# Kernel optimization log

Hardware: AMD Instinct MI355X
Metric: run time of the kernel (lower is better)

## Reference

```python
import jax, jax.numpy as jnp
import numpy as np

B, N, D, L = 64, 2047, 512, 4
T = D + 1        # token_dim = d + 1
H = 512          # hidden_dim
LN_EPS = 1e-5
ATTN_EPS = 1e-6


def setup_inputs() -> dict:
    key = jax.random.key(0)
    ks = jax.random.split(key, 10)
    s = 0.01  # matches xavier_uniform_ gain=0.01 small-init magnitude
    return dict(
        xs=jax.random.normal(ks[0], (B, N, D), jnp.float32),
        ys=jax.random.normal(ks[1], (B, N), jnp.float32),
        query_x=jax.random.normal(ks[2], (B, 1, D), jnp.float32),
        Wq=jax.random.normal(ks[3], (L, H, T), jnp.float32) * s,
        Wk=jax.random.normal(ks[4], (L, H, T), jnp.float32) * s,
        Wv=jax.random.normal(ks[5], (L, T, T), jnp.float32) * s,
        Wo=jax.random.normal(ks[6], (L, T, T), jnp.float32) * s,
        ln1_w=jnp.ones((L, T), jnp.float32),
        ln1_b=jnp.zeros((L, T), jnp.float32),
        ln2_w=jnp.ones((L, T), jnp.float32),
        ln2_b=jnp.zeros((L, T), jnp.float32),
        scale=jnp.ones((L,), jnp.float32),
        pred_w=jax.random.normal(ks[7], (1, T), jnp.float32) * 0.02,
    )


def _ln(x, w, b):
    m = jnp.mean(x, axis=-1, keepdims=True)
    v = jnp.var(x, axis=-1, keepdims=True)
    return (x - m) * jax.lax.rsqrt(v + LN_EPS) * w + b


def _l2norm(x):
    n = jnp.sqrt(jnp.sum(x * x, axis=-1, keepdims=True))
    return x / jnp.maximum(n, 1e-12)


def _forward(xs, ys, query_x, Wq, Wk, Wv, Wo, ln1_w, ln1_b, ln2_w, ln2_b, scale, pred_w):
    b = xs.shape[0]
    train_tokens = jnp.concatenate([xs, ys[..., None]], axis=-1)          # [B,N,T]
    query_token = jnp.concatenate([query_x, jnp.zeros((b, 1, 1), xs.dtype)], axis=-1)
    tokens = jnp.concatenate([train_tokens, query_token], axis=1)          # [B,N+1,T]

    def step(tok, p):
        wq, wk, wv, wo, w1, b1, w2, b2, sc = p
        x = _ln(tok, w1, b1)
        Q = jnp.einsum('bnt,ht->bnh', x, wq)
        K = jnp.einsum('bnt,ht->bnh', x, wk)
        V = jnp.einsum('bnt,ut->bnu', x, wv)
        Q = _l2norm(Q)
        K = _l2norm(K)
        s = jax.nn.softplus(sc)
        Qp = (jax.nn.elu(Q) + 1.0) * s
        Kp = jax.nn.elu(K) + 1.0
        KV = jnp.einsum('bnh,bnu->bhu', Kp, V)      # [B,H,T]
        Ksum = jnp.sum(Kp, axis=1)                  # [B,H]
        denom = jnp.einsum('bnh,bh->bn', Qp, Ksum)  # [B,N+1]
        attn = jnp.einsum('bnh,bhu->bnu', Qp, KV) / (denom[..., None] + ATTN_EPS)
        out = jnp.einsum('bnu,tu->bnt', attn, wo) * 0.1 + tok
        return _ln(out, w2, b2), None

    tokens, _ = jax.lax.scan(step, tokens, (Wq, Wk, Wv, Wo, ln1_w, ln1_b, ln2_w, ln2_b, scale))
    q_out = tokens[:, -1, :]                        # [B,T]
    return jnp.einsum('bt,ot->bo', q_out, pred_w)[..., 0]  # [B]


def reference(xs, ys, query_x, Wq, Wk, Wv, Wo, ln1_w, ln1_b, ln2_w, ln2_b, scale, pred_w):
    return _forward(xs, ys, query_x, Wq, Wk, Wv, Wo, ln1_w, ln1_b, ln2_w, ln2_b, scale, pred_w)
```

## Files before the change

kernel.cpp:

```cpp
#include <hip/hip_runtime.h>
#include <cstdint>
#include <cstddef>


typedef unsigned short u16;
typedef float f32x4 __attribute__((ext_vector_type(4)));
typedef unsigned short u16x8 __attribute__((ext_vector_type(8)));

#define P 576
#define NQK 1664
#define VTROWS 514
#define KVLD 640

__device__ __forceinline__ float bf2f(u16 s) {
    union { unsigned u; float f; } v; v.u = ((unsigned)s) << 16; return v.f;
}
__device__ __forceinline__ u16 f2bf(float f) {
    union { float f; unsigned u; } v; v.f = f;
    unsigned r = v.u + 0x7FFF + ((v.u >> 16) & 1);
    return (u16)(r >> 16);
}
__device__ __forceinline__ float wredsum(float v) {
#pragma unroll
    for (int o = 32; o > 0; o >>= 1) v += __shfl_xor(v, o, 64);
    return v;
}
__device__ __forceinline__ f32x4 mfma_16x16x32_bf16(u16x8 a, u16x8 b, f32x4 c) {
    asm volatile("v_mfma_f32_16x16x32_bf16 %0, %1, %2, %0"
                 : "+v"(c) : "v"(a), "v"(b));
    return c;
}
__device__ __forceinline__ void gload_lds16(const u16* g, u16* l) {
    __builtin_amdgcn_global_load_lds(
        (const __attribute__((address_space(1))) void*)g,
        (__attribute__((address_space(3))) void*)l, 16, 0, 0);
}

__global__ __launch_bounds__(256) void k_build_tokens(
    const float* __restrict__ xs, const float* __restrict__ ys,
    const float* __restrict__ qx, u16* __restrict__ tok,
    float* __restrict__ meanb, float* __restrict__ rstdb)
{
    long row = (long)blockIdx.x * 4 + (threadIdx.x >> 6);
    int lane = threadIdx.x & 63;
    int b = (int)(row >> 11), n = (int)(row & 2047);
    const float* src = (n < 2047) ? xs + ((long)(b * 2047 + n)) * 512
                                  : qx + (long)b * 512;
    float4 f0 = *(const float4*)(src + lane * 8);
    float4 f1 = *(const float4*)(src + lane * 8 + 4);
    float y = (n < 2047) ? ys[(long)b * 2047 + n] : 0.f;
    float v[8] = {f0.x, f0.y, f0.z, f0.w, f1.x, f1.y, f1.z, f1.w};
    float s = 0.f, sq = 0.f;
#pragma unroll
    for (int j = 0; j < 8; j++) { s += v[j]; sq += v[j] * v[j]; }
    if (lane == 0) { s += y; sq += y * y; }
    s = wredsum(s); sq = wredsum(sq);
    u16x8 o;
#pragma unroll
    for (int j = 0; j < 8; j++) o[j] = f2bf(v[j]);
    *(u16x8*)(tok + row * P + lane * 8) = o;
    if (lane < 8) {
        u16x8 z8 = {0,0,0,0,0,0,0,0};
        if (lane == 0) z8[0] = f2bf(y);
        *(u16x8*)(tok + row * P + 512 + lane * 8) = z8;
    }
    if (lane == 0) {
        float m = s * (1.f / 513.f);
        float var = sq * (1.f / 513.f) - m * m;
        meanb[row] = m;
        rstdb[row] = 1.f / sqrtf(var + 1e-5f);
    }
}

__global__ __launch_bounds__(256) void k_prep_wcat(
    const float* __restrict__ wq, const float* __restrict__ wk,
    const float* __restrict__ wv, const float* __restrict__ ln1w,
    u16* __restrict__ wcat)
{
    long idx = (long)blockIdx.x * 256 + threadIdx.x;
    if (idx >= 4L * NQK * P) return;
    int t = (int)(idx % P);
    long rem = idx / P;
    int r = (int)(rem % NQK);
    int l = (int)(rem / NQK);
    float v = 0.f;
    if (t < 513) {
        float wsc = ln1w[l * 513 + t];
        if (r < 512)       v = wq[((long)l * 512 + r) * 513 + t] * wsc;
        else if (r < 1024) v = wk[((long)l * 512 + (r - 512)) * 513 + t] * wsc;
        else if (r < 1537) v = wv[((long)l * 513 + (r - 1024)) * 513 + t] * wsc;
    }
    wcat[idx] = f2bf(v);
}

__global__ __launch_bounds__(256) void k_prep_wo(
    const float* __restrict__ wo, u16* __restrict__ wop)
{
    long idx = (long)blockIdx.x * 256 + threadIdx.x;
    if (idx >= 4L * P * P) return;
    int u = (int)(idx % P);
    long rem = idx / P;
    int t = (int)(rem % P);
    int l = (int)(rem / P);
    float v = (t < 513 && u < 513) ? wo[((long)l * 513 + t) * 513 + u] : 0.f;
    wop[idx] = f2bf(v);
}

__global__ __launch_bounds__(256) void k_prep_sums(
    const float* __restrict__ wq, const float* __restrict__ wk,
    const float* __restrict__ wv, const float* __restrict__ ln1w,
    const float* __restrict__ ln1b, float* __restrict__ s1, float* __restrict__ s2)
{
    int id = blockIdx.x * 4 + (threadIdx.x >> 6);
    int lane = threadIdx.x & 63;
    int l = id / NQK, r = id % NQK;
    float a1 = 0.f, a2 = 0.f;
    for (int t = lane; t < 513; t += 64) {
        float wc = 0.f;
        if (r < 512)       wc = wq[((long)l * 512 + r) * 513 + t];
        else if (r < 1024) wc = wk[((long)l * 512 + (r - 512)) * 513 + t];
        else if (r < 1537) wc = wv[((long)l * 513 + (r - 1024)) * 513 + t];
        a1 += ln1w[l * 513 + t] * wc;
        a2 += ln1b[l * 513 + t] * wc;
    }
    a1 = wredsum(a1); a2 = wredsum(a2);
    if (lane == 0) { s1[id] = a1; s2[id] = a2; }
}

__global__ __launch_bounds__(256) void k_ln2(
    const u16* __restrict__ z, u16* __restrict__ tok,
    const float* __restrict__ w, const float* __restrict__ bia,
    float* __restrict__ meanb, float* __restrict__ rstdb)
{
    long row = (long)blockIdx.x * 4 + (threadIdx.x >> 6);
    int lane = threadIdx.x & 63;
    const u16* zp = z + row * P;
    u16* tp = tok + row * P;
    u16x8 a0 = *(const u16x8*)(zp + lane * 8);
    u16x8 a1 = {0,0,0,0,0,0,0,0};
    if (lane < 8) a1 = *(const u16x8*)(zp + 512 + lane * 8);
    float v0[8], v1[8];
#pragma unroll
    for (int j = 0; j < 8; j++) v0[j] = bf2f(a0[j]);
#pragma unroll
    for (int j = 0; j < 8; j++) v1[j] = (lane < 8) ? bf2f(a1[j]) : 0.f;
    float s = 0.f, sq = 0.f;
#pragma unroll
    for (int j = 0; j < 8; j++) { s += v0[j]; sq += v0[j] * v0[j]; }
#pragma unroll
    for (int j = 0; j < 8; j++) { s += v1[j]; sq += v1[j] * v1[j]; }
    s = wredsum(s); sq = wredsum(sq);
    float mean = s * (1.f / 513.f);
    float var = sq * (1.f / 513.f) - mean * mean;
    float rstd = 1.f / sqrtf(var + 1e-5f);
    float so = 0.f, so2 = 0.f;
    u16x8 o0;
    float of0[8];
#pragma unroll
    for (int j = 0; j < 8; j++) {
        int t = lane * 8 + j;
        of0[j] = (v0[j] - mean) * rstd * w[t] + bia[t];
        so += of0[j]; so2 += of0[j] * of0[j];
        o0[j] = f2bf(of0[j]);
    }
    float of1[8];
#pragma unroll
    for (int j = 0; j < 8; j++) {
        int t = 512 + lane * 8 + j;
        float ov = 0.f;
        if (lane < 8 && t < 513) ov = (v1[j] - mean) * rstd * w[t] + bia[t];
        of1[j] = ov;
        so += ov; so2 += ov * ov;
    }
    so = wredsum(so); so2 = wredsum(so2);
    *(u16x8*)(tp + lane * 8) = o0;
    if (lane < 8) {
        u16x8 o1;
#pragma unroll
        for (int j = 0; j < 8; j++) o1[j] = f2bf(of1[j]);
        *(u16x8*)(tp + 512 + lane * 8) = o1;
    }
    if (lane == 0) {
        float m2 = so * (1.f / 513.f);
        float v2 = so2 * (1.f / 513.f) - m2 * m2;
        meanb[row] = m2;
        rstdb[row] = 1.f / sqrtf(v2 + 1e-5f);
    }
}

__global__ __launch_bounds__(256) void k_qknorm(
    u16* __restrict__ qkv, float* __restrict__ rkout,
    const float* __restrict__ scale, int l)
{
    long row = (long)blockIdx.x * 4 + (threadIdx.x >> 6);
    int lane = threadIdx.x & 63;
    float s = log1pf(expf(scale[l]));
    u16* rowp = qkv + row * NQK;
    u16x8 q8 = *(const u16x8*)(rowp + lane * 8);
    u16x8 k8 = *(const u16x8*)(rowp + 512 + lane * 8);
    float qf[8];
    float sqv = 0.f, skv = 0.f;
#pragma unroll
    for (int j = 0; j < 8; j++) { qf[j] = bf2f(q8[j]); sqv += qf[j] * qf[j]; }
#pragma unroll
    for (int j = 0; j < 8; j++) { float kf = bf2f(k8[j]); skv += kf * kf; }
    sqv = wredsum(sqv); skv = wredsum(skv);
    float rnq = 1.f / fmaxf(sqrtf(sqv), 1e-12f);
    float rnk = 1.f / fmaxf(sqrtf(skv), 1e-12f);
    u16x8 o;
#pragma unroll
    for (int j = 0; j < 8; j++) {
        float q = qf[j] * rnq;
        float qp = (q > 0.f) ? (q + 1.f) : expf(q);
        o[j] = f2bf(qp * s);
    }
    *(u16x8*)(rowp + lane * 8) = o;
    if (lane == 0) rkout[row] = rnk;
}

__global__ __launch_bounds__(256) void k_trans(
    const u16* __restrict__ qkv, const float* __restrict__ rk,
    u16* __restrict__ kpt)
{
    int ct = blockIdx.x;
    long r0 = (long)blockIdx.y * 64;
    int b = (int)(r0 >> 11);
    int nloc = (int)(r0 & 2047);
    int tid = threadIdx.x;
    int r = tid >> 2;
    int c0 = (tid & 3) * 16;
    __shared__ u16 T[64 * 80];
    const u16* src = qkv + (r0 + r) * NQK + 512 + ct * 64 + c0;
    u16x8 a = *(const u16x8*)src;
    u16x8 d = *(const u16x8*)(src + 8);
    float rkv = rk[r0 + r];
#pragma unroll
    for (int j = 0; j < 8; j++) {
        float kv = bf2f(a[j]) * rkv; kv = (kv > 0.f) ? kv + 1.f : expf(kv);
        T[(c0 + j) * 80 + r] = f2bf(kv);
    }
#pragma unroll
    for (int j = 0; j < 8; j++) {
        float kv = bf2f(d[j]) * rkv; kv = (kv > 0.f) ? kv + 1.f : expf(kv);
        T[(c0 + 8 + j) * 80 + r] = f2bf(kv);
    }
    __syncthreads();
    int orow = tid >> 2;
    int oc0 = (tid & 3) * 16;
    u16x8 w0 = *(const u16x8*)&T[orow * 80 + oc0];
    u16x8 w1 = *(const u16x8*)&T[orow * 80 + oc0 + 8];
    u16* dst = kpt + ((long)b * 512 + ct * 64 + orow) * 2048 + nloc + oc0;
    *(u16x8*)dst = w0;
    *(u16x8*)(dst + 8) = w1;
}

__global__ __launch_bounds__(512) void k_extract_ksum(
    const u16* __restrict__ kvh, float* __restrict__ ksum)
{
    int b = blockIdx.x, h = threadIdx.x;
    ksum[(long)b * 512 + h] = bf2f(kvh[((long)b * 512 + h) * KVLD + 513]);
}

__global__ __launch_bounds__(256) void k_denom(
    const u16* __restrict__ qkv, const float* __restrict__ ksum,
    float* __restrict__ denom)
{
    long row = (long)blockIdx.x * 4 + (threadIdx.x >> 6);
    int lane = threadIdx.x & 63;
    int b = (int)(row >> 11);
    u16x8 q = *(const u16x8*)(qkv + row * NQK + lane * 8);
    const float* ks = ksum + (long)b * 512 + lane * 8;
    float acc = 0.f;
#pragma unroll
    for (int j = 0; j < 8; j++) acc += bf2f(q[j]) * ks[j];
    acc = wredsum(acc);
    if (lane == 0) denom[row] = acc;
}

__global__ void k_predict(const u16* __restrict__ tok, const float* __restrict__ pw,
                          float* __restrict__ out)
{
    int b = blockIdx.x;
    int lane = threadIdx.x;
    const u16* rp = tok + ((long)b * 2048 + 2047) * P;
    float acc = 0.f;
    for (int t = lane; t < 513; t += 64) acc += bf2f(rp[t]) * pw[t];
    acc = wredsum(acc);
    if (lane == 0) out[b] = acc;
}

#define QN 1664

#define QSTAGE(DB, HALF, K0)                                                   \
    {                                                                          \
        _Pragma("unroll")                                                      \
        for (int j = 0; j < 2; j++) {                                          \
            int row_ = j * 64 + srow;                                          \
            const u16* src_;                                                   \
            if ((HALF) < 2) {                                                  \
                src_ = Ag + (long)(m0 + (HALF) * 128 + row_) * 576 + (K0) + colsw; \
            } else {                                                           \
                int gc_ = n0 + ((HALF) - 2) * 128 + row_;                      \
                if (gc_ >= QN) gc_ = QN - 1;                                   \
                src_ = Bg + (long)gc_ * 576 + (K0) + colsw;                    \
            }                                                                  \
            gload_lds16(src_, S + (DB) * 32768 + (HALF) * 8192 + j * 4096 + w * 512); \
        }                                                                      \
    }

#define QLDA(AH)                                                               \
    _Pragma("unroll")                                                          \
    for (int m_ = 0; m_ < 4; m_++) {                                           \
        int rr_ = wr * 64 + m_ * 16 + (lane & 15);                             \
        _Pragma("unroll")                                                      \
        for (int ks_ = 0; ks_ < 2; ks_++)                                      \
            af[m_][ks_] = *(const u16x8*)&Bc[(AH) * 8192 + rr_ * 64 +          \
                          ((ks_ * 32 + (lane >> 4) * 8) ^ swz)];               \
    }

#define QLDB(BH)                                                               \
    _Pragma("unroll")                                                          \
    for (int n_ = 0; n_ < 2; n_++) {                                           \
        int cc_ = wc * 32 + n_ * 16 + (lane & 15);                             \
        _Pragma("unroll")                                                      \
        for (int ks_ = 0; ks_ < 2; ks_++)                                      \
            bf[n_][ks_] = *(const u16x8*)&Bc[16384 + (BH) * 8192 + cc_ * 64 +  \
                          ((ks_ * 32 + (lane >> 4) * 8) ^ swz)];               \
    }

#define QPHASE(AH, BH, RDA, RDB, SHALF)                                        \
    __builtin_amdgcn_sched_barrier(0);                                         \
    if (RDA) { QLDA(AH) }                                                      \
    if (RDB) { QLDB(BH) }                                                      \
    QSTAGE(nb, SHALF, k1)                                                      \
    asm volatile("s_waitcnt vmcnt(4)" ::: "memory");                           \
    __builtin_amdgcn_s_barrier();                                              \
    __builtin_amdgcn_s_setprio(1);                                             \
    _Pragma("unroll")                                                          \
    for (int m_ = 0; m_ < 4; m_++)                                             \
        _Pragma("unroll")                                                      \
        for (int n_ = 0; n_ < 2; n_++) {                                       \
            acc[AH][BH][m_][n_] =                                              \
                mfma_16x16x32_bf16(af[m_][0], bf[n_][0], acc[AH][BH][m_][n_]); \
            acc[AH][BH][m_][n_] =                                              \
                mfma_16x16x32_bf16(af[m_][1], bf[n_][1], acc[AH][BH][m_][n_]); \
        }                                                                      \
    __builtin_amdgcn_s_setprio(0);                                             \
    __builtin_amdgcn_s_barrier();

__global__ __launch_bounds__(512, 2) void k_qkv8(
    const u16* __restrict__ Ag, const u16* __restrict__ Bg, u16* __restrict__ C,
    const float* __restrict__ meanb, const float* __restrict__ rstdb,
    const float* __restrict__ s1l, const float* __restrict__ s2l,
    u16* __restrict__ VT)
{
    extern __shared__ u16 S[];
    int id = blockIdx.x;
    int lin = (id & 7) * 448 + (id >> 3);
    int mt = lin / 7, nt = lin - mt * 7;
    int m0 = mt * 256, n0 = nt * 256;
    int tid = threadIdx.x, lane = tid & 63, w = tid >> 6;
    int wr = w >> 2, wc = w & 3;

    float* auxp = (float*)(S + 65536);
    if (tid < 256) {
        auxp[tid] = meanb[(long)m0 + tid];
        auxp[256 + tid] = rstdb[(long)m0 + tid];
    } else {
        int t = tid - 256;
        int gc = n0 + t; if (gc >= QN) gc = QN - 1;
        auxp[512 + t] = s1l[gc];
        auxp[768 + t] = s2l[gc];
    }

    int srow = (w << 3) + (lane >> 3);
    int colsw = ((lane & 7) << 3) ^ ((lane >> 3) << 3);
    int swz = (lane & 7) << 3;

    f32x4 acc[2][2][4][2];
#pragma unroll
    for (int a_ = 0; a_ < 2; a_++)
#pragma unroll
    for (int b_ = 0; b_ < 2; b_++)
#pragma unroll
    for (int m_ = 0; m_ < 4; m_++)
#pragma unroll
    for (int n_ = 0; n_ < 2; n_++) {
        acc[a_][b_][m_][n_][0] = 0.f; acc[a_][b_][m_][n_][1] = 0.f;
        acc[a_][b_][m_][n_][2] = 0.f; acc[a_][b_][m_][n_][3] = 0.f;
    }
    u16x8 af[4][2], bf[2][2];

    QSTAGE(0, 0, 0) QSTAGE(0, 2, 0) QSTAGE(0, 3, 0) QSTAGE(0, 1, 0)
    asm volatile("s_waitcnt vmcnt(4)" ::: "memory");
    __builtin_amdgcn_s_barrier();

    for (int kt = 0; kt < 9; ++kt) {
        u16* Bc = S + (kt & 1) * 32768;
        int nb = (kt & 1) ^ 1;
        int k1 = (kt >= 8 ? 8 : kt + 1) * 64;
        QPHASE(0, 0, 1, 1, 0)
        QPHASE(0, 1, 0, 1, 2)
        QPHASE(1, 1, 1, 0, 3)
        QPHASE(1, 0, 0, 1, 1)
    }
    asm volatile("s_waitcnt vmcnt(0)" ::: "memory");
    __builtin_amdgcn_s_barrier();

    if (n0 < 1024) {
#pragma unroll
        for (int ah = 0; ah < 2; ah++)
#pragma unroll
        for (int bh = 0; bh < 2; bh++)
#pragma unroll
        for (int m_ = 0; m_ < 4; m_++)
#pragma unroll
        for (int n_ = 0; n_ < 2; n_++) {
            int lr0 = ah * 128 + wr * 64 + m_ * 16 + ((lane >> 4) << 2);
            int lc = bh * 128 + wc * 32 + n_ * 16 + (lane & 15);
            float s1c = auxp[512 + lc], s2c = auxp[768 + lc];
#pragma unroll
            for (int r_ = 0; r_ < 4; r_++) {
                int lr = lr0 + r_;
                float v = auxp[256 + lr] * (acc[ah][bh][m_][n_][r_]
                          - auxp[lr] * s1c) + s2c;
                S[lr * 256 + (lc ^ ((lr & 7) << 3))] = f2bf(v);
            }
        }
        __syncthreads();
#pragma unroll
        for (int i = 0; i < 16; i++) {
            int g = i * 512 + tid;
            int row = g >> 5, c0 = (g & 31) * 8;
            *(u16x8*)&C[(long)(m0 + row) * 1664 + n0 + c0] =
                *(const u16x8*)&S[row * 256 + (c0 ^ ((row & 7) << 3))];
        }
    } else {
        int u0 = n0 - 1024, b = m0 >> 11, nloc = m0 & 2047;
#pragma unroll
        for (int ah = 0; ah < 2; ah++)
#pragma unroll
        for (int bh = 0; bh < 2; bh++)
#pragma unroll
        for (int m_ = 0; m_ < 4; m_++)
#pragma unroll
        for (int n_ = 0; n_ < 2; n_++) {
            int lr0 = ah * 128 + wr * 64 + m_ * 16 + ((lane >> 4) << 2);
            int lc = bh * 128 + wc * 32 + n_ * 16 + (lane & 15);
            float s1c = auxp[512 + lc], s2c = auxp[768 + lc];
#pragma unroll
            for (int r_ = 0; r_ < 4; r_++) {
                int lr = lr0 + r_;
                float v = auxp[256 + lr] * (acc[ah][bh][m_][n_][r_]
                          - auxp[lr] * s1c) + s2c;
                S[lc * 256 + (lr ^ ((lc & 7) << 3))] = f2bf(v);
            }
        }
        __syncthreads();
        const u16x8 ones = {0x3F80,0x3F80,0x3F80,0x3F80,0x3F80,0x3F80,0x3F80,0x3F80};
#pragma unroll
        for (int i = 0; i < 16; i++) {
            int g = i * 512 + tid;
            int ur = g >> 5, t0 = (g & 31) * 8;
            int u = u0 + ur;
            if (u < VTROWS) {
                u16x8 vv;
                if (u == 513) vv = ones;
                else vv = *(const u16x8*)&S[ur * 256 + (t0 ^ ((ur & 7) << 3))];
                *(u16x8*)&VT[((long)b * VTROWS + u) * 2048 + nloc + t0] = vv;
            }
        }
    }
}

__global__ __launch_bounds__(256) void k_gemm_bt(
    const u16* __restrict__ A, const u16* __restrict__ Bt, u16* __restrict__ C,
    int M, int N, int K, int lda, int ldb, int ldc,
    long sA, long sB, long sC,
    const float* __restrict__ aux1, const float* __restrict__ aux2,
    const float* __restrict__ aux3, const float* __restrict__ aux4,
    long sAux, const u16* __restrict__ Res,
    float cscale, int mode, int r1, int padw,
    int ntm, int ntn, int nbz,
    u16* __restrict__ VT, int vtbase)
{
    int G = ntm * ntn * nbz;
    int id = blockIdx.x;
    int lin = (id & 7) * (G >> 3) + (id >> 3);
    int per = ntm * ntn;
    int bz = lin / per;
    int rem = lin - bz * per;
    int mt = rem / ntn;
    int nt = rem - mt * ntn;
    int m0 = mt * 128, n0 = nt * 128;

    A += (long)bz * sA; Bt += (long)bz * sB; C += (long)bz * sC;
    int tid = threadIdx.x, lane = tid & 63, w = tid >> 6;
    int wr = w >> 1, wc = w & 1;
    __shared__ u16 ldsbuf[2 * 128 * 64];
    u16* Als = ldsbuf;
    u16* Bls = ldsbuf + 128 * 64;
    __shared__ float auxR0[128], auxR1[128], auxA1[128];
    __shared__ float auxC0[128], auxC1[128], auxB1[128];

    if (tid < 128) {
        int gr = m0 + tid; if (gr >= M) gr = M - 1;
        float r0v = cscale, r1v = 0.f, a1v = 0.f;
        if (mode == 1) {
            const float* d1 = aux1 + (long)bz * sAux;
            r0v = cscale / (d1[gr] + 1e-6f);
        } else if (mode == 3) { r0v = aux1[gr]; r1v = aux2[gr]; }
        if (r1) a1v = bf2f(A[(long)gr * lda + K]);
        auxR0[tid] = r0v; auxR1[tid] = r1v; auxA1[tid] = a1v;
    } else {
        int t = tid - 128;
        int gc = n0 + t; if (gc >= N) gc = N - 1;
        float c0v = 0.f, c1v = 0.f, b1v = 0.f;
        if (mode == 3) { c0v = aux3[gc]; c1v = aux4[gc]; }
        if (r1) b1v = bf2f(Bt[(long)gc * ldb + K]);
        auxC0[t] = c0v; auxC1[t] = c1v; auxB1[t] = b1v;
    }

    f32x4 acc[4][4];
#pragma unroll
    for (int m = 0; m < 4; m++)
#pragma unroll
        for (int n = 0; n < 4; n++) { acc[m][n][0]=0.f; acc[m][n][1]=0.f; acc[m][n][2]=0.f; acc[m][n][3]=0.f; }

    int srow = lane >> 3;
    int scol = (lane & 7) * 8;
    int scolsw = scol ^ (srow << 3);
    int swz = (lane & 7) << 3;

    for (int k0 = 0; k0 < K; k0 += 64) {
#pragma unroll
        for (int i = 0; i < 4; i++) {
            int rt = (w * 4 + i) * 8 + srow;
            int gr = m0 + rt; gr = (gr < M) ? gr : (M - 1);
            gload_lds16(A + (long)gr * lda + k0 + scolsw, &Als[(w * 4 + i) * 512]);
        }
#pragma unroll
        for (int i = 0; i < 4; i++) {
            int rt = (w * 4 + i) * 8 + srow;
            int gc = n0 + rt; gc = (gc < N) ? gc : (N - 1);
            gload_lds16(Bt + (long)gc * ldb + k0 + scolsw, &Bls[(w * 4 + i) * 512]);
        }
        __syncthreads();
#pragma unroll
        for (int ks = 0; ks < 2; ks++) {
            u16x8 af[4], bfv[4];
#pragma unroll
            for (int m = 0; m < 4; m++) {
                int row = wr * 64 + m * 16 + (lane & 15);
                af[m] = *(const u16x8*)&Als[row * 64 + ((ks * 32 + (lane >> 4) * 8) ^ swz)];
            }
#pragma unroll
            for (int n = 0; n < 4; n++) {
                int col = wc * 64 + n * 16 + (lane & 15);
                bfv[n] = *(const u16x8*)&Bls[col * 64 + ((ks * 32 + (lane >> 4) * 8) ^ swz)];
            }
#pragma unroll
            for (int m = 0; m < 4; m++)
#pragma unroll
                for (int n = 0; n < 4; n++)
                    acc[m][n] = mfma_16x16x32_bf16(af[m], bfv[n], acc[m][n]);
        }
        __syncthreads();
    }

    bool isvt = (VT != nullptr) && (n0 >= vtbase);

    if (Res) {
        const u16* Rp = Res + (long)bz * sC;
#pragma unroll
        for (int i = 0; i < 8; i++) {
            int lrow = i * 16 + (tid >> 4);
            int lcol = (tid & 15) * 8;
            long gr = m0 + lrow; if (gr > (long)M - 1) gr = M - 1;
            long gcol = (long)n0 + lcol;
            long mx = (long)ldc - 8; if (gcol > mx) gcol = mx;
            *(u16x8*)&ldsbuf[lrow * 128 + lcol] = *(const u16x8*)&Rp[gr * ldc + gcol];
        }
        __syncthreads();
    }

    asm volatile("s_nop 7\n\ts_nop 7" ::: );

    if (!isvt) {
#pragma unroll
        for (int m = 0; m < 4; m++) {
            int lrbase = wr * 64 + m * 16 + ((lane >> 4) << 2);
#pragma unroll
            for (int n = 0; n < 4; n++) {
                int lc = wc * 64 + n * 16 + (lane & 15);
                float c0v = auxC0[lc], c1v = auxC1[lc], b1v = auxB1[lc];
#pragma unroll
                for (int r = 0; r < 4; r++) {
                    int lr = lrbase + r;
                    float wv = acc[m][n][r] + auxA1[lr] * b1v;
                    float v;
                    if (mode == 3) v = auxR1[lr] * (wv - auxR0[lr] * c0v) + c1v;
                    else {
                        v = wv * auxR0[lr];
                        if (Res) v += bf2f(ldsbuf[lr * 128 + lc]);
                    }
                    ldsbuf[lr * 128 + lc] = f2bf(v);
                }
            }
        }
        __syncthreads();

        int lcol = (tid & 15) * 8;
        int gc0 = n0 + lcol;
        bool colok = padw || (gc0 + 8 <= N);
#pragma unroll
        for (int i = 0; i < 8; i++) {
            int lrow = i * 16 + (tid >> 4);
            int gr = m0 + lrow;
            if (gr < M && colok) {
                *(u16x8*)&C[(long)gr * ldc + gc0] = *(const u16x8*)&ldsbuf[lrow * 128 + lcol];
            }
        }
    } else {
        int u0 = n0 - vtbase;
        int b = m0 >> 11;
        int nloc = m0 & 2047;
#pragma unroll
        for (int m = 0; m < 4; m++) {
            int lrbase = wr * 64 + m * 16 + ((lane >> 4) << 2);
#pragma unroll
            for (int n = 0; n < 4; n++) {
                int lc = wc * 64 + n * 16 + (lane & 15);
                float c0v = auxC0[lc], c1v = auxC1[lc];
#pragma unroll
                for (int r = 0; r < 4; r++) {
                    int lr = lrbase + r;
                    float wv = acc[m][n][r];
                    float v = (mode == 3) ? (auxR1[lr] * (wv - auxR0[lr] * c0v) + c1v)
                                          : (wv * auxR0[lr]);
                    ldsbuf[lc * 128 + (lr ^ ((lc & 7) << 3))] = f2bf(v);
                }
            }
        }
        __syncthreads();

        int nc = (tid & 15) * 8;
        const u16x8 ones = {0x3F80,0x3F80,0x3F80,0x3F80,0x3F80,0x3F80,0x3F80,0x3F80};
#pragma unroll
        for (int i = 0; i < 8; i++) {
            int ur = i * 16 + (tid >> 4);
            int u = u0 + ur;
            if (u < VTROWS) {
                u16x8 vv;
                if (u == 513) vv = ones;
                else vv = *(const u16x8*)&ldsbuf[ur * 128 + (nc ^ ((ur & 7) << 3))];
                *(u16x8*)&VT[((long)b * VTROWS + u) * 2048 + nloc + nc] = vv;
            }
        }
    }
}

extern "C" void kernel_launch(void* const* d_in, const int* in_sizes, int n_in,
                              void* d_out, int out_size, void* d_ws, size_t ws_size,
                              hipStream_t stream)
{
    const float* xs    = (const float*)d_in[0];
    const float* ys    = (const float*)d_in[1];
    const float* qx    = (const float*)d_in[2];
    const float* Wq    = (const float*)d_in[3];
    const float* Wk    = (const float*)d_in[4];
    const float* Wv    = (const float*)d_in[5];
    const float* Wo    = (const float*)d_in[6];
    const float* ln1w  = (const float*)d_in[7];
    const float* ln1b  = (const float*)d_in[8];
    const float* ln2w  = (const float*)d_in[9];
    const float* ln2b  = (const float*)d_in[10];
    const float* scale = (const float*)d_in[11];
    const float* predw = (const float*)d_in[12];
    float* out = (float*)d_out;

    char* ws = (char*)d_ws;
    u16*   tok   = (u16*)(ws + 0L);
    u16*   buf1  = (u16*)(ws + 150994944L);
    u16*   qkv   = (u16*)(ws + 301989888L);
    u16*   kpt   = (u16*)(ws + 738197504L);
    u16*   kvh   = (u16*)(ws + 872415232L);
    float* denom = (float*)(ws + 914358272L);
    float* meanb = (float*)(ws + 914882560L);
    float* rstdb = (float*)(ws + 915406848L);
    float* ksum  = (float*)(ws + 915931136L);
    u16*   wcat  = (u16*)(ws + 916062208L);
    u16*   wop   = (u16*)(ws + 923729920L);
    float* s1    = (float*)(ws + 926384128L);
    float* s2    = (float*)(ws + 926410752L);
    float* rkb   = (float*)(ws + 301465600L);
    u16*   w2t   = kpt;

    static bool attr_done = false;
    if (!attr_done) {
        (void)hipFuncSetAttribute((const void*)k_qkv8,
            hipFuncAttributeMaxDynamicSharedMemorySize, 135168);
        attr_done = true;
    }

    k_build_tokens<<<32768, 256, 0, stream>>>(xs, ys, qx, tok, meanb, rstdb);
    {
        long n1 = 4L * NQK * P;
        k_prep_wcat<<<(int)((n1 + 255) / 256), 256, 0, stream>>>(Wq, Wk, Wv, ln1w, wcat);
        long n2 = 4L * P * P;
        k_prep_wo<<<(int)((n2 + 255) / 256), 256, 0, stream>>>(Wo, wop);
        k_prep_sums<<<1664, 256, 0, stream>>>(Wq, Wk, Wv, ln1w, ln1b, s1, s2);
    }

    for (int l = 0; l < 4; l++) {
        k_qkv8<<<3584, 512, 135168, stream>>>(tok, wcat + (long)l * NQK * P, qkv,
            meanb, rstdb, s1 + l * NQK, s2 + l * NQK, buf1);
        k_qknorm<<<32768, 256, 0, stream>>>(qkv, rkb, scale, l);
        {
            dim3 g(8, 2048, 1);
            k_trans<<<g, 256, 0, stream>>>(qkv, rkb, kpt);
        }
        k_gemm_bt<<<1280, 256, 0, stream>>>(kpt, buf1, kvh,
            512, VTROWS, 2048, 2048, 2048, KVLD,
            512L * 2048, (long)VTROWS * 2048, 512L * KVLD,
            nullptr, nullptr, nullptr, nullptr, 0, nullptr, 1.f, 0, 0, 1,
            4, 5, 64, nullptr, 1 << 30);
        k_extract_ksum<<<64, 512, 0, stream>>>(kvh, ksum);
        k_denom<<<32768, 256, 0, stream>>>(qkv, ksum, denom);
        k_gemm_bt<<<1280, 256, 0, stream>>>(wop + (long)l * P * P, kvh, w2t,
            576, 512, 512, P, KVLD, 512,
            0, 512L * KVLD, 576L * 512,
            nullptr, nullptr, nullptr, nullptr, 0, nullptr, 1.f, 0, 1, 0,
            5, 4, 64, nullptr, 1 << 30);
        k_gemm_bt<<<5120, 256, 0, stream>>>(qkv, w2t, buf1,
            2048, P, 512, NQK, 512, P,
            2048L * NQK, 576L * 512, 2048L * P,
            denom, nullptr, nullptr, nullptr, 2048, tok,
            0.1f, 1, 0, 0, 16, 5, 64, nullptr, 1 << 30);
        k_ln2<<<32768, 256, 0, stream>>>(buf1, tok, ln2w + l * 513, ln2b + l * 513,
                                         meanb, rstdb);
    }
    k_predict<<<64, 64, 0, stream>>>(tok, predw, out);
}
```

Baseline: 3.494 ms.

## Software-pipeline LDS fragment loads ahead of MFMA phases in QKV GEMM

Restructures the QKV GEMM main loop so LDS reads of the next A/B fragments are issued before or after the MFMA batches, using separate register sets (afA/afB, b0a/b0b). This hides LDS latency behind MFMA work, and the loop is manually unrolled by two tiles to alternate buffers. It costs more VGPRs for the extra fragment arrays, which could cause spills or lower occupancy under launch_bounds(512,2). It also adds lgkmcnt waits before each barrier.

```diff
diff --git a/kernel.cpp b/kernel.cpp
--- a/kernel.cpp
+++ b/kernel.cpp
@@ -308,45 +308,56 @@
         }                                                                      \
     }
 
-#define QLDA(AH)                                                               \
-    _Pragma("unroll")                                                          \
-    for (int m_ = 0; m_ < 4; m_++) {                                           \
-        int rr_ = wr * 64 + m_ * 16 + (lane & 15);                             \
-        _Pragma("unroll")                                                      \
-        for (int ks_ = 0; ks_ < 2; ks_++)                                      \
-            af[m_][ks_] = *(const u16x8*)&Bc[(AH) * 8192 + rr_ * 64 +          \
-                          ((ks_ * 32 + (lane >> 4) * 8) ^ swz)];               \
-    }
-
-#define QLDB(BH)                                                               \
-    _Pragma("unroll")                                                          \
-    for (int n_ = 0; n_ < 2; n_++) {                                           \
-        int cc_ = wc * 32 + n_ * 16 + (lane & 15);                             \
-        _Pragma("unroll")                                                      \
-        for (int ks_ = 0; ks_ < 2; ks_++)                                      \
-            bf[n_][ks_] = *(const u16x8*)&Bc[16384 + (BH) * 8192 + cc_ * 64 +  \
-                          ((ks_ * 32 + (lane >> 4) * 8) ^ swz)];               \
-    }
-
-#define QPHASE(AH, BH, RDA, RDB, SHALF)                                        \
-    __builtin_amdgcn_sched_barrier(0);                                         \
-    if (RDA) { QLDA(AH) }                                                      \
-    if (RDB) { QLDB(BH) }                                                      \
-    QSTAGE(nb, SHALF, k1)                                                      \
-    asm volatile("s_waitcnt vmcnt(4)" ::: "memory");                           \
-    __builtin_amdgcn_s_barrier();                                              \
+#define QLGKM0 asm volatile("s_waitcnt lgkmcnt(0)" ::: "memory");
+#define QVM4   asm volatile("s_waitcnt vmcnt(4)" ::: "memory");
+#define QBAR   __builtin_amdgcn_s_barrier();                                   \
+               __builtin_amdgcn_sched_barrier(0);
+
+#define QMFMA(AF, BF, AH, BH)                                                  \
     __builtin_amdgcn_s_setprio(1);                                             \
     _Pragma("unroll")                                                          \
     for (int m_ = 0; m_ < 4; m_++)                                             \
         _Pragma("unroll")                                                      \
         for (int n_ = 0; n_ < 2; n_++) {                                       \
             acc[AH][BH][m_][n_] =                                              \
-                mfma_16x16x32_bf16(af[m_][0], bf[n_][0], acc[AH][BH][m_][n_]); \
+                mfma_16x16x32_bf16(AF[m_][0], BF[n_][0], acc[AH][BH][m_][n_]); \
             acc[AH][BH][m_][n_] =                                              \
-                mfma_16x16x32_bf16(af[m_][1], bf[n_][1], acc[AH][BH][m_][n_]); \
+                mfma_16x16x32_bf16(AF[m_][1], BF[n_][1], acc[AH][BH][m_][n_]); \
         }                                                                      \
-    __builtin_amdgcn_s_setprio(0);                                             \
-    __builtin_amdgcn_s_barrier();
+    __builtin_amdgcn_s_setprio(0);
+
+#define QLDAF(DST, BUF, AHALF)                                                 \
+    _Pragma("unroll")                                                          \
+    for (int m_ = 0; m_ < 4; m_++) {                                           \
+        int rr_ = wr * 64 + m_ * 16 + (lane & 15);                             \
+        _Pragma("unroll")                                                      \
+        for (int ks_ = 0; ks_ < 2; ks_++)                                      \
+            DST[m_][ks_] = *(const u16x8*)&S[(BUF) * 32768 + (AHALF) * 8192 +  \
+                rr_ * 64 + ((ks_ * 32 + (lane >> 4) * 8) ^ swz)];              \
+    }
+
+#define QLDBF(DST, BUF, BHALF)                                                 \
+    _Pragma("unroll")                                                          \
+    for (int n_ = 0; n_ < 2; n_++) {                                           \
+        int cc_ = wc * 32 + n_ * 16 + (lane & 15);                             \
+        _Pragma("unroll")                                                      \
+        for (int ks_ = 0; ks_ < 2; ks_++)                                      \
+            DST[n_][ks_] = *(const u16x8*)&S[(BUF) * 32768 + 16384 +           \
+                (BHALF) * 8192 + cc_ * 64 + ((ks_ * 32 + (lane >> 4) * 8) ^ swz)]; \
+    }
+
+#define QTILE(PI, B0CUR, B0NXT, K1, DOLAST)                                    \
+     QSTAGE((PI) ^ 1, 0, K1) QLGKM0 QVM4 QBAR                          \
+    QMFMA(afA, B0CUR, 0, 0)                                                    \
+    QLDBF(bf1, PI, 1)                                                          \
+     QSTAGE((PI) ^ 1, 2, K1) QLGKM0 QVM4 QBAR                          \
+    QMFMA(afA, bf1, 0, 1)                                                      \
+    QLDAF(afB, PI, 1)                                                          \
+     QSTAGE((PI) ^ 1, 3, K1) QLGKM0 QVM4 QBAR                          \
+    QMFMA(afB, bf1, 1, 1)                                                      \
+     QSTAGE((PI) ^ 1, 1, K1) QLGKM0 QVM4 QBAR                          \
+    QMFMA(afB, B0CUR, 1, 0)                                                    \
+    if (DOLAST) { QLDAF(afA, (PI) ^ 1, 0) QLDBF(B0NXT, (PI) ^ 1, 0) }
 
 __global__ __launch_bounds__(512, 2) void k_qkv8(
     const u16* __restrict__ Ag, const u16* __restrict__ Bg, u16* __restrict__ C,
@@ -389,21 +400,22 @@
         acc[a_][b_][m_][n_][0] = 0.f; acc[a_][b_][m_][n_][1] = 0.f;
         acc[a_][b_][m_][n_][2] = 0.f; acc[a_][b_][m_][n_][3] = 0.f;
     }
-    u16x8 af[4][2], bf[2][2];
+    u16x8 afA[4][2], afB[4][2], bf1[2][2], b0a[2][2], b0b[2][2];
 
     QSTAGE(0, 0, 0) QSTAGE(0, 2, 0) QSTAGE(0, 3, 0) QSTAGE(0, 1, 0)
-    asm volatile("s_waitcnt vmcnt(4)" ::: "memory");
+    QVM4
     __builtin_amdgcn_s_barrier();
-
-    for (int kt = 0; kt < 9; ++kt) {
-        u16* Bc = S + (kt & 1) * 32768;
-        int nb = (kt & 1) ^ 1;
-        int k1 = (kt >= 8 ? 8 : kt + 1) * 64;
-        QPHASE(0, 0, 1, 1, 0)
-        QPHASE(0, 1, 0, 1, 2)
-        QPHASE(1, 1, 1, 0, 3)
-        QPHASE(1, 0, 0, 1, 1)
-    }
+    QLDAF(afA, 0, 0) QLDBF(b0a, 0, 0)
+
+#pragma unroll 1
+    for (int it = 0; it < 4; ++it) {
+        int k1a = it * 128 + 64;
+        int k1b = it * 128 + 128;
+        QTILE(0, b0a, b0b, k1a, 1)
+        QTILE(1, b0b, b0a, k1b, 1)
+    }
+    QTILE(0, b0a, b0b, 512, 0)
+
     asm volatile("s_waitcnt vmcnt(0)" ::: "memory");
     __builtin_amdgcn_s_barrier();
 
```

Result: slower. 3.600 ms (+3.0%).
